# Kernel tuning notes

Measured on AMD Instinct MI355X. Metric: run time of the kernel, lower is better.

Reference implementation:

```python
import jax, jax.numpy as jnp
import numpy as np

DT = 0.5
TAU = 10.0
ALPHA = DT / TAU
GAMMA_MULT = 1.0


def setup_inputs() -> dict:
    key = jax.random.key(0)
    k1, k2, k3 = jax.random.split(key, 3)
    T, B, IN, N = 512, 128, 64, 1024
    H = 2 * N
    x = jax.random.normal(k1, (T, B, IN), dtype=jnp.float32)
    hidden0 = jax.random.uniform(k2, (B, H), dtype=jnp.float32)
    # wAttractor: fixed [H, H] ring-attractor weight matrix (generate_alpha_matrix stand-in)
    w_attractor = 0.01 * jax.random.normal(k3, (H, H), dtype=jnp.float32)
    # input_to_vel: Linear(IN, 1, bias=False), initialized to ones (trainable)
    w_in = jnp.ones((1, IN), dtype=jnp.float32)
    return {"x": x, "hidden0": hidden0, "w_attractor": w_attractor, "w_in": w_in}


def reference(x, hidden0, w_attractor, w_in):
    H = w_attractor.shape[0]
    n = H // 2
    # vel_to_ring frozen params: weight = gamma (shape [H,1]), bias = ones
    gamma = GAMMA_MULT * jnp.concatenate([-jnp.ones(n, x.dtype), jnp.ones(n, x.dtype)])
    # i2h for all timesteps at once: vel = x @ w_in.T -> [T,B,1]; i2h = vel*gamma + 1
    vel = jnp.einsum('tbi,oi->tbo', x, w_in)          # [T, B, 1]
    i2h = vel * gamma[None, None, :] + 1.0            # [T, B, H]

    def step(h, i2h_t):
        h2h = h @ w_attractor                          # [B, H]
        h_new = (1.0 - ALPHA) * h + ALPHA * jax.nn.relu(i2h_t + h2h)
        return h_new, h_new

    hT, acts = jax.lax.scan(step, hidden0, i2h)        # acts: [T, B, H]
    return acts, hT
```

## Files before the change

### kernel.cpp

```cpp
#include <hip/hip_runtime.h>

#define H_DIM   2048
#define N_HALF  1024
#define B_SZ    128
#define T_STEPS 512
#define IN_DIM  64
#define ALPHA_F 0.05f
#define OMA_F   0.95f

typedef __bf16 bf16x8 __attribute__((ext_vector_type(8)));
typedef float  f32x4  __attribute__((ext_vector_type(4)));
typedef unsigned int u32x4 __attribute__((ext_vector_type(4)));

__device__ __forceinline__ unsigned short f2bf(float f) {
    union { float f; unsigned int u; } v; v.f = f;
    unsigned int u = v.u;
    u += 0x7FFFu + ((u >> 16) & 1u);
    return (unsigned short)(u >> 16);
}

__global__ void wf_kernel(const float* __restrict__ W, unsigned short* __restrict__ Wf) {
    __shared__ float tile[64][65];
    const int jb = blockIdx.x * 64;
    const int kb = blockIdx.y * 64;
    const int t  = threadIdx.y * 64 + threadIdx.x;
    const int tx = threadIdx.x, ty = threadIdx.y;
    #pragma unroll
    for (int r = ty; r < 64; r += 4)
        tile[r][tx] = W[(size_t)(kb + r) * H_DIM + jb + tx];
    __syncthreads();
    #pragma unroll
    for (int cc = 0; cc < 2; ++cc) {
        const int c  = t * 2 + cc;
        const int jj = c >> 3;
        const int kc = c & 7;
        const int j  = jb + jj;
        const int k0 = kb + kc * 8;
        unsigned short v[8];
        #pragma unroll
        for (int e = 0; e < 8; ++e)
            v[e] = f2bf(tile[kc * 8 + e][jj]);
        const int ks = k0 >> 5;
        const int q4 = (k0 >> 3) & 3;
        const size_t dst = (size_t)(j >> 6) * 131072 +
                           ((size_t)(ks * 4 + q4) * 64 + (j & 63)) * 8;
        *reinterpret_cast<u32x4*>(Wf + dst) = *reinterpret_cast<u32x4*>(v);
    }
}

__global__ void vel_kernel(const float* __restrict__ x, const float* __restrict__ w_in,
                           float* __restrict__ vel) {
    const int tb = blockIdx.x * blockDim.x + threadIdx.x;
    if (tb >= T_STEPS * B_SZ) return;
    const float* xp = x + (size_t)tb * IN_DIM;
    float s = 0.f;
    #pragma unroll
    for (int i = 0; i < IN_DIM; i += 4) {
        float4 xv = *reinterpret_cast<const float4*>(xp + i);
        float4 wv = *reinterpret_cast<const float4*>(w_in + i);
        s += xv.x * wv.x + xv.y * wv.y + xv.z * wv.z + xv.w * wv.w;
    }
    vel[tb] = s;
}

__global__ void hbf_init_kernel(const float* __restrict__ h0, unsigned short* __restrict__ hbf) {
    const int i = blockIdx.x * blockDim.x + threadIdx.x;
    hbf[i] = f2bf(h0[i]);
}

__global__ __launch_bounds__(512, 1) void ring_coop_kernel(
        const unsigned short* __restrict__ Wf,
        unsigned short* __restrict__ hbf0,
        unsigned short* __restrict__ hbf1,
        const float* __restrict__ vel,
        const float* __restrict__ hidden0,
        float* __restrict__ acts,
        float* __restrict__ outT,
        unsigned* __restrict__ flags) {
    __shared__ __align__(16) unsigned char A_lds[65536];
    __shared__ __align__(16) f32x4 pacc[256];
    __shared__ __align__(16) float hbuf[16][64];

    const int tid = threadIdx.x;
    const int bid = blockIdx.x;
    const int colg = (bid & 7) * 4 + ((bid >> 3) & 3);
    const int rowg = bid >> 5;
    const int colbase = colg * 64;
    const int rowbase = rowg * 16;

    const int lane = tid & 63, w = tid >> 6;
    const int colq = w & 3, khalf = w >> 2;
    const int r16 = lane & 15, q4 = lane >> 4;
    const int j = colbase + colq * 16 + r16;
    const float gamma = (j < N_HALF) ? -1.0f : 1.0f;

    const int srow = lane >> 3;
    const int kcl  = lane & 7;

    unsigned* rflags = flags + rowg * 128;

    const unsigned short* bgbase = Wf + (size_t)colg * 131072
                                   + (size_t)(khalf * 128 + q4) * 512
                                   + (size_t)(colq * 16 + r16) * 8;
    bf16x8 Breg[32];
    #pragma unroll
    for (int s = 0; s < 32; ++s)
        Breg[s] = *reinterpret_cast<const bf16x8*>(bgbase + (size_t)s * 2048);

    f32x4 hreg = {0.f, 0.f, 0.f, 0.f};
    if (khalf == 0) {
        #pragma unroll
        for (int i = 0; i < 4; ++i)
            hreg[i] = hidden0[(size_t)(rowbase + q4 * 4 + i) * H_DIM + j];
    }

    const int xe = r16 ^ q4;
    const int xo = xe ^ 4;

    const int cg0 = (colg + 1 + w) & 31;
    const int cgA = cg0, cgB = (cg0 + 8) & 31, cgC = (cg0 + 16) & 31, cgD = (cg0 + 24) & 31;
    const int pollcg = (cg0 + 8 * (lane & 3)) & 31;

    for (int t = 0; t < T_STEPS; ++t) {
        const unsigned short* hin  = (t & 1) ? hbf1 : hbf0;
        unsigned short*       hout = (t & 1) ? hbf0 : hbf1;
        const float* vel_t = vel + (size_t)t * B_SZ;
        float* acts_t = acts + (size_t)t * B_SZ * H_DIM;

        f32x4 vel4 = {0.f, 0.f, 0.f, 0.f};
        if (khalf == 0)
            vel4 = *reinterpret_cast<const f32x4*>(vel_t + rowbase + q4 * 4);

        for (;;) {
            int ok = 1;
            if (lane < 4) {
                unsigned v = __hip_atomic_load(rflags + pollcg * 4,
                                 __ATOMIC_RELAXED, __HIP_MEMORY_SCOPE_AGENT);
                ok = (v >= (unsigned)t);
            }
            if (__all(ok)) break;
            __builtin_amdgcn_s_sleep(1);
        }
        asm volatile("" ::: "memory");

        {
            const unsigned short* base = hin + (size_t)(rowbase + srow) * H_DIM + kcl * 8;
            u32x4 a0, a1, b0, b1, c0, c1, d0, d1;
            const unsigned short* pA = base + cgA * 64;
            const unsigned short* pB = base + cgB * 64;
            const unsigned short* pC = base + cgC * 64;
            const unsigned short* pD = base + cgD * 64;
            asm volatile("global_load_dwordx4 %0, %1, off sc0 sc1" : "=v"(a0) : "v"(pA));
            asm volatile("global_load_dwordx4 %0, %1, off sc0 sc1" : "=v"(a1) : "v"(pA + 8 * H_DIM));
            asm volatile("global_load_dwordx4 %0, %1, off sc0 sc1" : "=v"(b0) : "v"(pB));
            asm volatile("global_load_dwordx4 %0, %1, off sc0 sc1" : "=v"(b1) : "v"(pB + 8 * H_DIM));
            asm volatile("global_load_dwordx4 %0, %1, off sc0 sc1" : "=v"(c0) : "v"(pC));
            asm volatile("global_load_dwordx4 %0, %1, off sc0 sc1" : "=v"(c1) : "v"(pC + 8 * H_DIM));
            asm volatile("global_load_dwordx4 %0, %1, off sc0 sc1" : "=v"(d0) : "v"(pD));
            asm volatile("global_load_dwordx4 %0, %1, off sc0 sc1" : "=v"(d1) : "v"(pD + 8 * H_DIM));
            asm volatile("s_waitcnt vmcnt(0)" ::: "memory");
            __builtin_amdgcn_sched_barrier(0);
            const int lo_sw = srow ^ kcl, hi_sw = (srow + 8) ^ kcl;
            *reinterpret_cast<u32x4*>(A_lds + (size_t)((cgA * 8 + kcl) * 16 + lo_sw) * 16) = a0;
            *reinterpret_cast<u32x4*>(A_lds + (size_t)((cgA * 8 + kcl) * 16 + hi_sw) * 16) = a1;
            *reinterpret_cast<u32x4*>(A_lds + (size_t)((cgB * 8 + kcl) * 16 + lo_sw) * 16) = b0;
            *reinterpret_cast<u32x4*>(A_lds + (size_t)((cgB * 8 + kcl) * 16 + hi_sw) * 16) = b1;
            *reinterpret_cast<u32x4*>(A_lds + (size_t)((cgC * 8 + kcl) * 16 + lo_sw) * 16) = c0;
            *reinterpret_cast<u32x4*>(A_lds + (size_t)((cgC * 8 + kcl) * 16 + hi_sw) * 16) = c1;
            *reinterpret_cast<u32x4*>(A_lds + (size_t)((cgD * 8 + kcl) * 16 + lo_sw) * 16) = d0;
            *reinterpret_cast<u32x4*>(A_lds + (size_t)((cgD * 8 + kcl) * 16 + hi_sw) * 16) = d1;
        }
        __syncthreads();

        const unsigned char* Abase = A_lds + (size_t)(khalf * 2048 + q4 * 16) * 16;
        f32x4 acc0 = {0.f,0.f,0.f,0.f}, acc1 = {0.f,0.f,0.f,0.f};
        f32x4 acc2 = {0.f,0.f,0.f,0.f}, acc3 = {0.f,0.f,0.f,0.f};
        #pragma unroll
        for (int s = 0; s < 32; s += 4) {
            bf16x8 a0 = *reinterpret_cast<const bf16x8*>(Abase +
                (size_t)((s + 0) * 64 + xe) * 16);
            bf16x8 a1 = *reinterpret_cast<const bf16x8*>(Abase +
                (size_t)((s + 1) * 64 + xo) * 16);
            bf16x8 a2 = *reinterpret_cast<const bf16x8*>(Abase +
                (size_t)((s + 2) * 64 + xe) * 16);
            bf16x8 a3 = *reinterpret_cast<const bf16x8*>(Abase +
                (size_t)((s + 3) * 64 + xo) * 16);
            acc0 = __builtin_amdgcn_mfma_f32_16x16x32_bf16(a0, Breg[s + 0], acc0, 0, 0, 0);
            acc1 = __builtin_amdgcn_mfma_f32_16x16x32_bf16(a1, Breg[s + 1], acc1, 0, 0, 0);
            acc2 = __builtin_amdgcn_mfma_f32_16x16x32_bf16(a2, Breg[s + 2], acc2, 0, 0, 0);
            acc3 = __builtin_amdgcn_mfma_f32_16x16x32_bf16(a3, Breg[s + 3], acc3, 0, 0, 0);
        }
        f32x4 psum = (acc0 + acc1) + (acc2 + acc3);

        if (khalf == 1) pacc[colq * 64 + lane] = psum;
        __syncthreads();
        if (khalf == 0) {
            const f32x4 h2h = psum + pacc[colq * 64 + lane];
            #pragma unroll
            for (int i = 0; i < 4; ++i) {
                const int row = rowbase + q4 * 4 + i;
                const float pre = fmaf(vel4[i], gamma, 1.0f) + h2h[i];
                const float hn = OMA_F * hreg[i] + ALPHA_F * fmaxf(pre, 0.0f);
                hreg[i] = hn;
                hbuf[q4 * 4 + i][colq * 16 + r16] = hn;
                acts_t[(size_t)row * H_DIM + j] = hn;
                if (t == T_STEPS - 1)
                    outT[(size_t)row * H_DIM + j] = hn;
            }
        }
        __syncthreads();

        if (tid >= 256 && tid < 384) {
            const int t2 = tid - 256;
            const int row2 = t2 >> 3, c8 = (t2 & 7) * 8;
            unsigned pk[4];
            #pragma unroll
            for (int e = 0; e < 4; ++e)
                pk[e] = (unsigned)f2bf(hbuf[row2][c8 + 2 * e]) |
                        ((unsigned)f2bf(hbuf[row2][c8 + 2 * e + 1]) << 16);
            u32x4 hv = {pk[0], pk[1], pk[2], pk[3]};
            unsigned short* dst = hout + (size_t)(rowbase + row2) * H_DIM + colbase + c8;
            asm volatile("global_store_dwordx4 %0, %1, off sc0 sc1"
                         :: "v"(dst), "v"(hv) : "memory");
            asm volatile("s_waitcnt vmcnt(0)" ::: "memory");
        }
        __syncthreads();
        if (tid == 0 && t < T_STEPS - 1)
            __hip_atomic_store(rflags + colg * 4, (unsigned)(t + 1),
                               __ATOMIC_RELAXED, __HIP_MEMORY_SCOPE_AGENT);
    }
}

__global__ __launch_bounds__(256) void step_kernel(
        const unsigned short* __restrict__ Wf,
        const unsigned short* __restrict__ hbf_in,
        unsigned short* __restrict__ hbf_out,
        const float* __restrict__ vel_t,
        const float* __restrict__ hprev,
        float* __restrict__ acts_t,
        float* __restrict__ outT) {
    const int lane = threadIdx.x & 63;
    const int w    = threadIdx.x >> 6;
    const int bid  = blockIdx.x;
    const int mg   = bid >> 7;
    const int n    = bid & 127;
    const int base_b = mg * 64 + w * 16;
    const int base_j = n * 16;
    const int r16  = lane & 15;
    const int q4   = lane >> 4;

    const int j = base_j + r16;
    const bf16x8* Ap = reinterpret_cast<const bf16x8*>(
        hbf_in + (size_t)(base_b + r16) * H_DIM + q4 * 8);
    const unsigned short* wslot = Wf + (size_t)(j >> 6) * 131072 + (size_t)(j & 63) * 8;

    f32x4 acc0 = {0.f, 0.f, 0.f, 0.f};
    f32x4 acc1 = {0.f, 0.f, 0.f, 0.f};
    #pragma unroll 8
    for (int kk = 0; kk < 32; ++kk) {
        bf16x8 a0 = Ap[kk * 4];
        bf16x8 a1 = Ap[kk * 4 + 128];
        bf16x8 b0 = *reinterpret_cast<const bf16x8*>(wslot + (size_t)(kk * 4 + q4) * 512);
        bf16x8 b1 = *reinterpret_cast<const bf16x8*>(wslot + (size_t)((kk + 32) * 4 + q4) * 512);
        acc0 = __builtin_amdgcn_mfma_f32_16x16x32_bf16(a0, b0, acc0, 0, 0, 0);
        acc1 = __builtin_amdgcn_mfma_f32_16x16x32_bf16(a1, b1, acc1, 0, 0, 0);
    }
    f32x4 h2h = acc0 + acc1;

    const float gamma = (j < N_HALF) ? -1.0f : 1.0f;
    const int brow0 = base_b + q4 * 4;
    #pragma unroll
    for (int i = 0; i < 4; ++i) {
        const int b = brow0 + i;
        const float v  = vel_t[b];
        const float hp = hprev[(size_t)b * H_DIM + j];
        const float pre = fmaf(v, gamma, 1.0f) + h2h[i];
        const float hn = OMA_F * hp + ALPHA_F * fmaxf(pre, 0.0f);
        acts_t[(size_t)b * H_DIM + j] = hn;
        hbf_out[(size_t)b * H_DIM + j] = f2bf(hn);
        if (outT) outT[(size_t)b * H_DIM + j] = hn;
    }
}

extern "C" void kernel_launch(void* const* d_in, const int* in_sizes, int n_in,
                              void* d_out, int out_size, void* d_ws, size_t ws_size,
                              hipStream_t stream) {
    const float* x       = (const float*)d_in[0];
    const float* hidden0 = (const float*)d_in[1];
    const float* w_attr  = (const float*)d_in[2];
    const float* w_in    = (const float*)d_in[3];

    float* acts = (float*)d_out;
    float* outT = acts + (size_t)T_STEPS * B_SZ * H_DIM;

    unsigned char* ws = (unsigned char*)d_ws;
    unsigned short* Wf   = (unsigned short*)ws;
    unsigned short* hbf0 = (unsigned short*)(ws + ((size_t)8 << 20));
    unsigned short* hbf1 = hbf0 + (size_t)B_SZ * H_DIM;
    float* vel = (float*)(ws + ((size_t)8 << 20) + (size_t)2 * B_SZ * H_DIM * 2);
    unsigned* flags = (unsigned*)(ws + ((size_t)8 << 20) + ((size_t)1 << 20) + (256 << 10));

    hipMemsetAsync(flags, 0, 4096, stream);
    wf_kernel<<<dim3(32, 32), dim3(64, 4), 0, stream>>>(w_attr, Wf);
    vel_kernel<<<(T_STEPS * B_SZ + 255) / 256, 256, 0, stream>>>(x, w_in, vel);
    hbf_init_kernel<<<(B_SZ * H_DIM + 255) / 256, 256, 0, stream>>>(hidden0, hbf0);

    void* args[] = {(void*)&Wf, (void*)&hbf0, (void*)&hbf1, (void*)&vel,
                    (void*)&hidden0, (void*)&acts, (void*)&outT, (void*)&flags};
    hipError_t rc = hipLaunchCooperativeKernel(
        reinterpret_cast<void*>(ring_coop_kernel),
        dim3(256), dim3(512), args, 0, stream);

    if (rc != hipSuccess) {
        for (int t = 0; t < T_STEPS; ++t) {
            const unsigned short* hin = (t & 1) ? hbf1 : hbf0;
            unsigned short* hout      = (t & 1) ? hbf0 : hbf1;
            const float* hprev = (t == 0) ? hidden0 : acts + (size_t)(t - 1) * B_SZ * H_DIM;
            step_kernel<<<256, 256, 0, stream>>>(
                Wf, hin, hout, vel + (size_t)t * B_SZ, hprev,
                acts + (size_t)t * B_SZ * H_DIM,
                (t == T_STEPS - 1) ? outT : nullptr);
        }
    }
}
```

Baseline: 1.878 ms.

## Publish per-wave h slices with per-wave flags, removing block barriers

Each of the four khalf==0 waves now packs its own 16x16 slice of the new hidden state to bf16, stores it, and raises its own readiness flag. This replaces the two extra __syncthreads and the single block-wide flag. Consumers poll 16 flags (four per column group) instead of four. The aim is to shorten the critical path of the per-timestep grid-wide dependency, at the cost of more flag traffic and more polling lanes.

```diff
diff --git a/kernel.cpp b/kernel.cpp
--- a/kernel.cpp
+++ b/kernel.cpp
@@ -79,7 +79,7 @@
         unsigned* __restrict__ flags) {
     __shared__ __align__(16) unsigned char A_lds[65536];
     __shared__ __align__(16) f32x4 pacc[256];
-    __shared__ __align__(16) float hbuf[16][64];
+    __shared__ __align__(16) float hbw[4][16][16];
 
     const int tid = threadIdx.x;
     const int bid = blockIdx.x;
@@ -119,7 +119,8 @@
 
     const int cg0 = (colg + 1 + w) & 31;
     const int cgA = cg0, cgB = (cg0 + 8) & 31, cgC = (cg0 + 16) & 31, cgD = (cg0 + 24) & 31;
-    const int pollcg = (cg0 + 8 * (lane & 3)) & 31;
+    const int pcg = (cg0 + 8 * (lane >> 2)) & 31;
+    const int pidx = pcg * 4 + (lane & 3);
 
     for (int t = 0; t < T_STEPS; ++t) {
         const unsigned short* hin  = (t & 1) ? hbf1 : hbf0;
@@ -133,8 +134,8 @@
 
         for (;;) {
             int ok = 1;
-            if (lane < 4) {
-                unsigned v = __hip_atomic_load(rflags + pollcg * 4,
+            if (lane < 16) {
+                unsigned v = __hip_atomic_load(rflags + pidx,
                                  __ATOMIC_RELAXED, __HIP_MEMORY_SCOPE_AGENT);
                 ok = (v >= (unsigned)t);
             }
@@ -194,6 +195,7 @@
 
         if (khalf == 1) pacc[colq * 64 + lane] = psum;
         __syncthreads();
+
         if (khalf == 0) {
             const f32x4 h2h = psum + pacc[colq * 64 + lane];
             #pragma unroll
@@ -202,32 +204,34 @@
                 const float pre = fmaf(vel4[i], gamma, 1.0f) + h2h[i];
                 const float hn = OMA_F * hreg[i] + ALPHA_F * fmaxf(pre, 0.0f);
                 hreg[i] = hn;
-                hbuf[q4 * 4 + i][colq * 16 + r16] = hn;
+                hbw[colq][q4 * 4 + i][r16] = hn;
                 acts_t[(size_t)row * H_DIM + j] = hn;
                 if (t == T_STEPS - 1)
                     outT[(size_t)row * H_DIM + j] = hn;
             }
-        }
-        __syncthreads();
-
-        if (tid >= 256 && tid < 384) {
-            const int t2 = tid - 256;
-            const int row2 = t2 >> 3, c8 = (t2 & 7) * 8;
-            unsigned pk[4];
-            #pragma unroll
-            for (int e = 0; e < 4; ++e)
-                pk[e] = (unsigned)f2bf(hbuf[row2][c8 + 2 * e]) |
-                        ((unsigned)f2bf(hbuf[row2][c8 + 2 * e + 1]) << 16);
-            u32x4 hv = {pk[0], pk[1], pk[2], pk[3]};
-            unsigned short* dst = hout + (size_t)(rowbase + row2) * H_DIM + colbase + c8;
-            asm volatile("global_store_dwordx4 %0, %1, off sc0 sc1"
-                         :: "v"(dst), "v"(hv) : "memory");
-            asm volatile("s_waitcnt vmcnt(0)" ::: "memory");
-        }
-        __syncthreads();
-        if (tid == 0 && t < T_STEPS - 1)
-            __hip_atomic_store(rflags + colg * 4, (unsigned)(t + 1),
-                               __ATOMIC_RELAXED, __HIP_MEMORY_SCOPE_AGENT);
+            if (t < T_STEPS - 1) {
+                asm volatile("s_waitcnt lgkmcnt(0)" ::: "memory");
+                __builtin_amdgcn_sched_barrier(0);
+                if (lane < 32) {
+                    const int prow = lane >> 1, phalf = lane & 1;
+                    const float* src = &hbw[colq][prow][phalf * 8];
+                    unsigned pk[4];
+                    #pragma unroll
+                    for (int e = 0; e < 4; ++e)
+                        pk[e] = (unsigned)f2bf(src[2 * e]) |
+                                ((unsigned)f2bf(src[2 * e + 1]) << 16);
+                    u32x4 hv = {pk[0], pk[1], pk[2], pk[3]};
+                    unsigned short* dst = hout + (size_t)(rowbase + prow) * H_DIM
+                                          + colbase + colq * 16 + phalf * 8;
+                    asm volatile("global_store_dwordx4 %0, %1, off sc0 sc1"
+                                 :: "v"(dst), "v"(hv) : "memory");
+                }
+                asm volatile("s_waitcnt vmcnt(0)" ::: "memory");
+                if (lane == 0)
+                    __hip_atomic_store(rflags + colg * 4 + colq, (unsigned)(t + 1),
+                                       __ATOMIC_RELAXED, __HIP_MEMORY_SCOPE_AGENT);
+            }
+        }
     }
 }
 
```

Measured after the change: 2.286 ms. +21.7%, slower.
